# Performance work log

Measured on AMD Instinct MI355X. Metric: run time of the kernel, lower is better.

Reference implementation:

```python
import jax, jax.numpy as jnp
import numpy as np

N, H, S, R, T = 32768, 512, 8, 64, 12

def setup_inputs() -> dict:
    key = jax.random.key(0)
    ks = jax.random.split(key, 7)
    scale = 1.0 / np.sqrt(H)
    return {
        "encodings": jax.random.normal(ks[0], (N, H), dtype=jnp.float32),
        "domain_encs": jax.random.normal(ks[1], (S, H), dtype=jnp.float32),
        "Us": jax.random.normal(ks[2], (S, H, R), dtype=jnp.float32) * scale,
        "W1": jax.random.normal(ks[3], (S, H, H), dtype=jnp.float32) * scale,
        "b1": jax.random.normal(ks[4], (S, H), dtype=jnp.float32) * 0.01,
        "W2": jax.random.normal(ks[5], (S, H, T), dtype=jnp.float32) * scale,
        "b2": jax.random.normal(ks[6], (S, T), dtype=jnp.float32) * 0.01,
    }

def reference(encodings, domain_encs, Us, W1, b1, W2, b2):
    # Mahalanobis soft routing. Original computes (p-mu) @ (U U^T) @ (p-mu)^T
    # and takes sqrt(diag) -- algebraically identical to project-then-square-sum.
    diff = encodings[None, :, :] - domain_encs[:, None, :]        # [S, N, H]
    proj = jnp.einsum('snh,shr->snr', diff, Us)                   # [S, N, R]
    dist = jnp.sqrt(jnp.sum(proj * proj, axis=-1))                # [S, N]
    alphas = jax.nn.softmax(-dist, axis=0)                        # softmax over sources

    # Per-source classifier: Dropout(eval=identity) -> ReLU -> Linear(H,H)
    # -> Dropout -> ReLU -> Linear(H,T) -> Sigmoid
    h0 = jax.nn.relu(encodings)                                   # [N, H]
    h1 = jax.nn.relu(jnp.einsum('nh,shk->snk', h0, W1) + b1[:, None, :])  # [S, N, H]
    out = jax.nn.sigmoid(jnp.einsum('snk,skt->snt', h1, W2) + b2[:, None, :])  # [S, N, T]

    # Softmax-weighted combine of expert outputs
    return jnp.sum(alphas[:, :, None] * out, axis=0)              # [N, T]
```

## Files before the change

### kernel.cpp

```cpp
#include <hip/hip_runtime.h>
#include <hip/hip_bf16.h>

typedef unsigned short u16;
typedef __bf16 bf16x8 __attribute__((ext_vector_type(8)));
typedef float f32x4 __attribute__((ext_vector_type(4)));

#define NROWS 32768
#define H 512
#define NS 8
#define NR 64
#define NT 12

#define WS_W1T   0
#define WS_UCT   4194304
#define WS_W2T   4718592
#define WS_CVEC  4849664
#define WS_ALPH  4851712

union BFU { __bf16 h; u16 u; };
__device__ __forceinline__ u16 f2bf(float v) { BFU b; b.h = (__bf16)v; return b.u; }

__device__ __forceinline__ void gload16(const u16* g, u16* l) {
  __builtin_amdgcn_global_load_lds(
      (const __attribute__((address_space(1))) unsigned int*)g,
      (__attribute__((address_space(3))) unsigned int*)l, 16, 0, 0);
}

__global__ __launch_bounds__(256) void prep(
    const float* __restrict__ W1, u16* __restrict__ W1T,
    const float* __restrict__ Us, u16* __restrict__ UcatT,
    const float* __restrict__ W2, u16* __restrict__ W2T,
    const float* __restrict__ mu, float* __restrict__ cvec) {
  __shared__ float tile[32][33];
  const int bid = blockIdx.x;
  const int tx = threadIdx.x, ty = threadIdx.y;
  if (bid < 2432) {
    const float* in; u16* out; int Rr, Cc, Cpad, b, r0, c0;
    if (bid < 2048) {
      in = W1; out = W1T; Rr = 512; Cc = 512; Cpad = 512;
      r0 = (bid & 15) * 32; c0 = ((bid >> 4) & 15) * 32; b = bid >> 8;
    } else if (bid < 2304) {
      int t2 = bid - 2048; in = Us; out = UcatT; Rr = 512; Cc = 64; Cpad = 64;
      r0 = (t2 & 15) * 32; c0 = ((t2 >> 4) & 1) * 32; b = t2 >> 5;
    } else {
      int t2 = bid - 2304; in = W2; out = W2T; Rr = 512; Cc = 12; Cpad = 16;
      r0 = (t2 & 15) * 32; c0 = 0; b = t2 >> 4;
    }
#pragma unroll
    for (int i = 0; i < 4; i++) {
      int r = r0 + ty + i * 8, c = c0 + tx;
      float v = 0.f;
      if (r < Rr && c < Cc) v = in[((size_t)b * Rr + r) * Cc + c];
      tile[ty + i * 8][tx] = v;
    }
    __syncthreads();
#pragma unroll
    for (int i = 0; i < 4; i++) {
      int c = c0 + ty + i * 8, r = r0 + tx;
      if (c < Cpad && r < Rr) out[((size_t)b * Cpad + c) * Rr + r] = f2bf(tile[tx][ty + i * 8]);
    }
  } else {
    const int tid = ty * 32 + tx;
    const int idx = (bid - 2432) * 4 + (tid >> 6);
    const int s = idx >> 6, r = idx & 63, t = tid & 63;
    float acc = 0.f;
#pragma unroll
    for (int k = t; k < H; k += 64) acc += mu[s * H + k] * Us[((size_t)s * H + k) * NR + r];
#pragma unroll
    for (int m = 32; m; m >>= 1) acc += __shfl_xor(acc, m, 64);
    if (t == 0) cvec[idx] = acc;
  }
}

__device__ __forceinline__ void stageW16(const u16* __restrict__ g, u16* l, int tid) {
#pragma unroll
  for (int i = 0; i < 4; i++) {
    int flat = tid + i * 256;
    int r = flat >> 5, u = flat & 31;
    gload16(g + (size_t)r * 512 + (u ^ (r & 7)) * 8, l + flat * 8);
  }
}

__global__ __launch_bounds__(256, 2) void routing(
    const float* __restrict__ enc, const u16* __restrict__ UcatT,
    const float* __restrict__ cvec, float* __restrict__ alphT) {
  __shared__ __align__(16) u16 Wst[3][32 * 256];
  __shared__ float distS[NS][64];
  __shared__ float cvS[512];

  const int tid = threadIdx.x;
  const int wave = tid >> 6, lane = tid & 63;
  const int lnm = lane & 15, lnq = lane >> 4;
  const int row0 = blockIdx.x * 64;

  cvS[tid] = cvec[tid];
  cvS[256 + tid] = cvec[256 + tid];

  bf16x8 afrag[16];
  {
    const float* rp = enc + (size_t)(row0 + wave * 16 + lnm) * H + lnq * 8;
#pragma unroll
    for (int ks = 0; ks < 16; ks++) {
      float4 x0 = *(const float4*)(rp + ks * 32);
      float4 x1 = *(const float4*)(rp + ks * 32 + 4);
      bf16x8 a;
      a[0] = (__bf16)x0.x; a[1] = (__bf16)x0.y; a[2] = (__bf16)x0.z; a[3] = (__bf16)x0.w;
      a[4] = (__bf16)x1.x; a[5] = (__bf16)x1.y; a[6] = (__bf16)x1.z; a[7] = (__bf16)x1.w;
      afrag[ks] = a;
    }
  }

  __syncthreads();

  stageW16(UcatT, Wst[0], tid);
  int cb = 0;
  float dsq[4] = {0.f, 0.f, 0.f, 0.f};
#pragma unroll 1
  for (int wcw = 0; wcw < 16; wcw++) {
    f32x4 acc[2] = {};
#pragma unroll
    for (int kh = 0; kh < 2; kh++) {
      const int q = wcw * 2 + kh;
      const int nb = (cb == 2) ? 0 : cb + 1;
      if (q + 1 < 32) {
        stageW16(UcatT + (size_t)((q + 1) >> 1) * 32 * 512 + ((q + 1) & 1) * 256, Wst[nb], tid);
        asm volatile("s_waitcnt vmcnt(4)" ::: "memory");
      } else {
        asm volatile("s_waitcnt vmcnt(0)" ::: "memory");
      }
      __builtin_amdgcn_s_barrier();
      const u16* buf = Wst[cb];
#pragma unroll
      for (int ks = 0; ks < 8; ks++) {
        const int uu = ((ks * 4 + lnq) ^ (lnm & 7)) * 8;
        bf16x8 b0 = *(const bf16x8*)&buf[lnm * 256 + uu];
        bf16x8 b1v = *(const bf16x8*)&buf[(16 + lnm) * 256 + uu];
        acc[0] = __builtin_amdgcn_mfma_f32_16x16x32_bf16(afrag[kh * 8 + ks], b0, acc[0], 0, 0, 0);
        acc[1] = __builtin_amdgcn_mfma_f32_16x16x32_bf16(afrag[kh * 8 + ks], b1v, acc[1], 0, 0, 0);
      }
      cb = nb;
    }
#pragma unroll
    for (int ct = 0; ct < 2; ct++) {
      float cv = cvS[wcw * 32 + ct * 16 + lnm];
#pragma unroll
      for (int g = 0; g < 4; g++) { float d = acc[ct][g] - cv; dsq[g] += d * d; }
    }
    if (wcw & 1) {
#pragma unroll
      for (int m = 1; m < 16; m <<= 1) {
#pragma unroll
        for (int g = 0; g < 4; g++) dsq[g] += __shfl_xor(dsq[g], m, 16);
      }
      if (lnm == 0) {
#pragma unroll
        for (int g = 0; g < 4; g++) distS[wcw >> 1][wave * 16 + lnq * 4 + g] = sqrtf(dsq[g]);
      }
#pragma unroll
      for (int g = 0; g < 4; g++) dsq[g] = 0.f;
    }
  }
  __syncthreads();
  if (tid < 64) {
    float dmin = distS[0][tid];
#pragma unroll
    for (int s = 1; s < NS; s++) dmin = fminf(dmin, distS[s][tid]);
    float den = 0.f, e[NS];
#pragma unroll
    for (int s = 0; s < NS; s++) { e[s] = __expf(dmin - distS[s][tid]); den += e[s]; }
    float inv = 1.f / den;
#pragma unroll
    for (int s = 0; s < NS; s++) alphT[(size_t)s * NROWS + row0 + tid] = e[s] * inv;
  }
}

#define H1STR 40

__device__ __forceinline__ const u16* chunk_base(const u16* W1g, int q) {
  return W1g + ((size_t)(q >> 5) * 512 + ((q >> 1) & 15) * 32) * 512 + (q & 1) * 256;
}

__global__ __launch_bounds__(256, 2) void moe_main(
    const float* __restrict__ enc, const u16* __restrict__ W1T,
    const u16* __restrict__ W2T, const float* __restrict__ alphT,
    const float* __restrict__ b1g, const float* __restrict__ b2g,
    float* __restrict__ out) {
  __shared__ __align__(16) u16 Wst[3][32 * 256];
  __shared__ __align__(16) u16 h1c[128 * H1STR];
  __shared__ float alphS[4][128];

  const int tid = threadIdx.x;
  const int wave = tid >> 6, lane = tid & 63;
  const int lnm = lane & 15, lnq = lane >> 4;
  const int rb = blockIdx.x >> 1, sg = blockIdx.x & 1;
  const int row0 = rb * 128, sbase = sg * 4;

#pragma unroll
  for (int i = 0; i < 2; i++) {
    int u = tid + i * 256, j = u >> 7, r = u & 127;
    alphS[j][r] = alphT[(size_t)(sbase + j) * NROWS + row0 + r];
  }

  float b2v[4];
#pragma unroll
  for (int j = 0; j < 4; j++) b2v[j] = (lnm < NT) ? b2g[(sbase + j) * NT + lnm] : 0.f;

  bf16x8 efrag[2][16];
#pragma unroll
  for (int t = 0; t < 2; t++) {
    const float* rp = enc + (size_t)(row0 + wave * 32 + t * 16 + lnm) * H + lnq * 8;
#pragma unroll
    for (int ks = 0; ks < 16; ks++) {
      float4 x0 = *(const float4*)(rp + ks * 32);
      float4 x1 = *(const float4*)(rp + ks * 32 + 4);
      bf16x8 a;
      a[0] = (__bf16)fmaxf(x0.x, 0.f); a[1] = (__bf16)fmaxf(x0.y, 0.f);
      a[2] = (__bf16)fmaxf(x0.z, 0.f); a[3] = (__bf16)fmaxf(x0.w, 0.f);
      a[4] = (__bf16)fmaxf(x1.x, 0.f); a[5] = (__bf16)fmaxf(x1.y, 0.f);
      a[6] = (__bf16)fmaxf(x1.z, 0.f); a[7] = (__bf16)fmaxf(x1.w, 0.f);
      efrag[t][ks] = a;
    }
  }

  __syncthreads();

  const u16* W1g = W1T + (size_t)sbase * 512 * 512;
  stageW16(chunk_base(W1g, 0), Wst[0], tid);
  int cb = 0;
  f32x4 acc[2][2];
  float fin[2][4] = {};
#pragma unroll 1
  for (int j = 0; j < 4; j++) {
    const int s = sbase + j;
    f32x4 oacc[2] = {};
#pragma unroll 1
    for (int wc = 0; wc < 16; wc++) {
      const int q = j * 32 + wc * 2;
      float4 bq0 = *(const float4*)&b1g[s * H + wc * 32 + lnq * 4];
      float4 bq1 = *(const float4*)&b1g[s * H + wc * 32 + 16 + lnq * 4];
      bf16x8 bw = *(const bf16x8*)&W2T[((size_t)s * 16 + lnm) * H + wc * 32 + lnq * 8];
      asm volatile("" ::: "memory");
      {
        const int nb = (cb == 2) ? 0 : cb + 1;
        stageW16(chunk_base(W1g, q + 1), Wst[nb], tid);
        asm volatile("s_waitcnt vmcnt(7)" ::: "memory");
        __builtin_amdgcn_s_barrier();
        const u16* buf = Wst[cb];
#pragma unroll
        for (int t = 0; t < 2; t++) {
          acc[t][0] = (f32x4){bq0.x, bq0.y, bq0.z, bq0.w};
          acc[t][1] = (f32x4){bq1.x, bq1.y, bq1.z, bq1.w};
        }
#pragma unroll
        for (int ks = 0; ks < 8; ks++) {
          const int uu = ((ks * 4 + lnq) ^ (lnm & 7)) * 8;
          bf16x8 w0 = *(const bf16x8*)&buf[lnm * 256 + uu];
          bf16x8 w1 = *(const bf16x8*)&buf[(16 + lnm) * 256 + uu];
#pragma unroll
          for (int t = 0; t < 2; t++) {
            acc[t][0] = __builtin_amdgcn_mfma_f32_16x16x32_bf16(w0, efrag[t][ks], acc[t][0], 0, 0, 0);
            acc[t][1] = __builtin_amdgcn_mfma_f32_16x16x32_bf16(w1, efrag[t][ks], acc[t][1], 0, 0, 0);
          }
        }
        cb = nb;
      }
      {
        const int nb = (cb == 2) ? 0 : cb + 1;
        if (q + 2 < 128) {
          stageW16(chunk_base(W1g, q + 2), Wst[nb], tid);
          asm volatile("s_waitcnt vmcnt(4)" ::: "memory");
        } else {
          asm volatile("s_waitcnt vmcnt(0)" ::: "memory");
        }
        __builtin_amdgcn_s_barrier();
        const u16* buf = Wst[cb];
#pragma unroll
        for (int ks = 0; ks < 8; ks++) {
          const int uu = ((ks * 4 + lnq) ^ (lnm & 7)) * 8;
          bf16x8 w0 = *(const bf16x8*)&buf[lnm * 256 + uu];
          bf16x8 w1 = *(const bf16x8*)&buf[(16 + lnm) * 256 + uu];
#pragma unroll
          for (int t = 0; t < 2; t++) {
            acc[t][0] = __builtin_amdgcn_mfma_f32_16x16x32_bf16(w0, efrag[t][8 + ks], acc[t][0], 0, 0, 0);
            acc[t][1] = __builtin_amdgcn_mfma_f32_16x16x32_bf16(w1, efrag[t][8 + ks], acc[t][1], 0, 0, 0);
          }
        }
        cb = nb;
      }
#pragma unroll
      for (int ct = 0; ct < 2; ct++) {
#pragma unroll
        for (int t = 0; t < 2; t++) {
          union { u16 u[4]; uint2 v; } pk;
          pk.u[0] = f2bf(fmaxf(acc[t][ct][0], 0.f));
          pk.u[1] = f2bf(fmaxf(acc[t][ct][1], 0.f));
          pk.u[2] = f2bf(fmaxf(acc[t][ct][2], 0.f));
          pk.u[3] = f2bf(fmaxf(acc[t][ct][3], 0.f));
          *(uint2*)&h1c[(wave * 32 + t * 16 + lnm) * H1STR + ct * 16 + lnq * 4] = pk.v;
        }
      }
      {
#pragma unroll
        for (int t = 0; t < 2; t++) {
          bf16x8 a2 = *(const bf16x8*)&h1c[(wave * 32 + t * 16 + lnm) * H1STR + lnq * 8];
          oacc[t] = __builtin_amdgcn_mfma_f32_16x16x32_bf16(a2, bw, oacc[t], 0, 0, 0);
        }
      }
    }
    {
#pragma unroll
      for (int t = 0; t < 2; t++) {
#pragma unroll
        for (int g = 0; g < 4; g++) {
          float sig = 1.f / (1.f + __expf(-(oacc[t][g] + b2v[j])));
          fin[t][g] += alphS[j][wave * 32 + t * 16 + lnq * 4 + g] * sig;
        }
      }
    }
  }
  if (lnm < NT) {
#pragma unroll
    for (int t = 0; t < 2; t++) {
#pragma unroll
      for (int g = 0; g < 4; g++) {
        int rg = row0 + wave * 32 + t * 16 + lnq * 4 + g;
        atomicAdd(&out[(size_t)rg * NT + lnm], fin[t][g]);
      }
    }
  }
}

extern "C" void kernel_launch(void* const* d_in, const int* in_sizes, int n_in,
                              void* d_out, int out_size, void* d_ws, size_t ws_size,
                              hipStream_t stream) {
  const float* enc = (const float*)d_in[0];
  const float* mu  = (const float*)d_in[1];
  const float* Us  = (const float*)d_in[2];
  const float* W1  = (const float*)d_in[3];
  const float* b1  = (const float*)d_in[4];
  const float* W2  = (const float*)d_in[5];
  const float* b2  = (const float*)d_in[6];
  float* out = (float*)d_out;
  char* ws = (char*)d_ws;
  u16* W1T    = (u16*)(ws + WS_W1T);
  u16* UcatT  = (u16*)(ws + WS_UCT);
  u16* W2T    = (u16*)(ws + WS_W2T);
  float* cvec = (float*)(ws + WS_CVEC);
  float* alphT = (float*)(ws + WS_ALPH);

  prep<<<2560, dim3(32, 8, 1), 0, stream>>>(W1, W1T, Us, UcatT, W2, W2T, mu, cvec);
  routing<<<512, 256, 0, stream>>>(enc, UcatT, cvec, alphT);
  hipMemsetAsync(out, 0, (size_t)out_size * sizeof(float), stream);
  moe_main<<<512, 256, 0, stream>>>(enc, W1T, W2T, alphT, b1, b2, out);
}
```

Measured before the change: 270.1 us.

## Split routing by source groups over 128-row tiles and move softmax into moe_main

```diff
diff --git a/kernel.cpp b/kernel.cpp
--- a/kernel.cpp
+++ b/kernel.cpp
@@ -15,7 +15,7 @@
 #define WS_UCT   4194304
 #define WS_W2T   4718592
 #define WS_CVEC  4849664
-#define WS_ALPH  4851712
+#define WS_DIST  4851712
 
 union BFU { __bf16 h; u16 u; };
 __device__ __forceinline__ u16 f2bf(float v) { BFU b; b.h = (__bf16)v; return b.u; }
@@ -81,24 +81,29 @@
   }
 }
 
+__device__ __forceinline__ const u16* rchunk(const u16* U, int rcol0, int q) {
+  return U + ((size_t)(rcol0 + (q >> 2) * 64 + ((q >> 1) & 1) * 32)) * 512 + (q & 1) * 256;
+}
+
 __global__ __launch_bounds__(256, 2) void routing(
     const float* __restrict__ enc, const u16* __restrict__ UcatT,
-    const float* __restrict__ cvec, float* __restrict__ alphT) {
+    const float* __restrict__ cvec, float* __restrict__ distT) {
   __shared__ __align__(16) u16 Wst[3][32 * 256];
-  __shared__ float distS[NS][64];
-  __shared__ float cvS[512];
+  __shared__ float cvS[256];
 
   const int tid = threadIdx.x;
   const int wave = tid >> 6, lane = tid & 63;
   const int lnm = lane & 15, lnq = lane >> 4;
-  const int row0 = blockIdx.x * 64;
-
-  cvS[tid] = cvec[tid];
-  cvS[256 + tid] = cvec[256 + tid];
-
-  bf16x8 afrag[16];
-  {
-    const float* rp = enc + (size_t)(row0 + wave * 16 + lnm) * H + lnq * 8;
+  const int rb = blockIdx.x >> 1, sg = blockIdx.x & 1;
+  const int row0 = rb * 128, sbase = sg * 4;
+  const int rcol0 = sbase * 64;
+
+  cvS[tid] = cvec[rcol0 + tid];
+
+  bf16x8 efrag[2][16];
+#pragma unroll
+  for (int t = 0; t < 2; t++) {
+    const float* rp = enc + (size_t)(row0 + wave * 32 + t * 16 + lnm) * H + lnq * 8;
 #pragma unroll
     for (int ks = 0; ks < 16; ks++) {
       float4 x0 = *(const float4*)(rp + ks * 32);
@@ -106,71 +111,68 @@
       bf16x8 a;
       a[0] = (__bf16)x0.x; a[1] = (__bf16)x0.y; a[2] = (__bf16)x0.z; a[3] = (__bf16)x0.w;
       a[4] = (__bf16)x1.x; a[5] = (__bf16)x1.y; a[6] = (__bf16)x1.z; a[7] = (__bf16)x1.w;
-      afrag[ks] = a;
+      efrag[t][ks] = a;
     }
   }
 
   __syncthreads();
 
-  stageW16(UcatT, Wst[0], tid);
+  stageW16(rchunk(UcatT, rcol0, 0), Wst[0], tid);
   int cb = 0;
-  float dsq[4] = {0.f, 0.f, 0.f, 0.f};
+  f32x4 acc[2][2];
 #pragma unroll 1
-  for (int wcw = 0; wcw < 16; wcw++) {
-    f32x4 acc[2] = {};
-#pragma unroll
-    for (int kh = 0; kh < 2; kh++) {
-      const int q = wcw * 2 + kh;
-      const int nb = (cb == 2) ? 0 : cb + 1;
-      if (q + 1 < 32) {
-        stageW16(UcatT + (size_t)((q + 1) >> 1) * 32 * 512 + ((q + 1) & 1) * 256, Wst[nb], tid);
-        asm volatile("s_waitcnt vmcnt(4)" ::: "memory");
-      } else {
-        asm volatile("s_waitcnt vmcnt(0)" ::: "memory");
-      }
-      __builtin_amdgcn_s_barrier();
-      const u16* buf = Wst[cb];
-#pragma unroll
-      for (int ks = 0; ks < 8; ks++) {
-        const int uu = ((ks * 4 + lnq) ^ (lnm & 7)) * 8;
-        bf16x8 b0 = *(const bf16x8*)&buf[lnm * 256 + uu];
-        bf16x8 b1v = *(const bf16x8*)&buf[(16 + lnm) * 256 + uu];
-        acc[0] = __builtin_amdgcn_mfma_f32_16x16x32_bf16(afrag[kh * 8 + ks], b0, acc[0], 0, 0, 0);
-        acc[1] = __builtin_amdgcn_mfma_f32_16x16x32_bf16(afrag[kh * 8 + ks], b1v, acc[1], 0, 0, 0);
-      }
-      cb = nb;
-    }
-#pragma unroll
-    for (int ct = 0; ct < 2; ct++) {
-      float cv = cvS[wcw * 32 + ct * 16 + lnm];
-#pragma unroll
-      for (int g = 0; g < 4; g++) { float d = acc[ct][g] - cv; dsq[g] += d * d; }
-    }
-    if (wcw & 1) {
-#pragma unroll
-      for (int m = 1; m < 16; m <<= 1) {
-#pragma unroll
-        for (int g = 0; g < 4; g++) dsq[g] += __shfl_xor(dsq[g], m, 16);
-      }
-      if (lnm == 0) {
-#pragma unroll
-        for (int g = 0; g < 4; g++) distS[wcw >> 1][wave * 16 + lnq * 4 + g] = sqrtf(dsq[g]);
-      }
-#pragma unroll
-      for (int g = 0; g < 4; g++) dsq[g] = 0.f;
-    }
-  }
-  __syncthreads();
-  if (tid < 64) {
-    float dmin = distS[0][tid];
-#pragma unroll
-    for (int s = 1; s < NS; s++) dmin = fminf(dmin, distS[s][tid]);
-    float den = 0.f, e[NS];
-#pragma unroll
-    for (int s = 0; s < NS; s++) { e[s] = __expf(dmin - distS[s][tid]); den += e[s]; }
-    float inv = 1.f / den;
-#pragma unroll
-    for (int s = 0; s < NS; s++) alphT[(size_t)s * NROWS + row0 + tid] = e[s] * inv;
+  for (int j = 0; j < 4; j++) {
+    float dsq[2] = {0.f, 0.f};
+#pragma unroll 1
+    for (int wc = 0; wc < 2; wc++) {
+#pragma unroll
+      for (int t = 0; t < 2; t++) { acc[t][0] = (f32x4){0,0,0,0}; acc[t][1] = (f32x4){0,0,0,0}; }
+#pragma unroll
+      for (int kh = 0; kh < 2; kh++) {
+        const int q = j * 4 + wc * 2 + kh;
+        const int nb = (cb == 2) ? 0 : cb + 1;
+        if (q + 1 < 16) {
+          stageW16(rchunk(UcatT, rcol0, q + 1), Wst[nb], tid);
+          asm volatile("s_waitcnt vmcnt(4)" ::: "memory");
+        } else {
+          asm volatile("s_waitcnt vmcnt(0)" ::: "memory");
+        }
+        __builtin_amdgcn_s_barrier();
+        const u16* buf = Wst[cb];
+#pragma unroll
+        for (int ks = 0; ks < 8; ks++) {
+          const int uu = ((ks * 4 + lnq) ^ (lnm & 7)) * 8;
+          bf16x8 w0 = *(const bf16x8*)&buf[lnm * 256 + uu];
+          bf16x8 w1 = *(const bf16x8*)&buf[(16 + lnm) * 256 + uu];
+#pragma unroll
+          for (int t = 0; t < 2; t++) {
+            acc[t][0] = __builtin_amdgcn_mfma_f32_16x16x32_bf16(w0, efrag[t][kh * 8 + ks], acc[t][0], 0, 0, 0);
+            acc[t][1] = __builtin_amdgcn_mfma_f32_16x16x32_bf16(w1, efrag[t][kh * 8 + ks], acc[t][1], 0, 0, 0);
+          }
+        }
+        cb = nb;
+      }
+#pragma unroll
+      for (int ct = 0; ct < 2; ct++) {
+        float4 cv4 = *(const float4*)&cvS[j * 64 + wc * 32 + ct * 16 + lnq * 4];
+#pragma unroll
+        for (int t = 0; t < 2; t++) {
+          float d0 = acc[t][ct][0] - cv4.x, d1 = acc[t][ct][1] - cv4.y;
+          float d2 = acc[t][ct][2] - cv4.z, d3 = acc[t][ct][3] - cv4.w;
+          dsq[t] += d0 * d0 + d1 * d1 + d2 * d2 + d3 * d3;
+        }
+      }
+    }
+#pragma unroll
+    for (int t = 0; t < 2; t++) {
+      dsq[t] += __shfl_xor(dsq[t], 16, 64);
+      dsq[t] += __shfl_xor(dsq[t], 32, 64);
+    }
+    if (lnq == 0) {
+#pragma unroll
+      for (int t = 0; t < 2; t++)
+        distT[(size_t)(sbase + j) * NROWS + row0 + wave * 32 + t * 16 + lnm] = sqrtf(dsq[t]);
+    }
   }
 }
 
@@ -182,7 +184,7 @@
 
 __global__ __launch_bounds__(256, 2) void moe_main(
     const float* __restrict__ enc, const u16* __restrict__ W1T,
-    const u16* __restrict__ W2T, const float* __restrict__ alphT,
+    const u16* __restrict__ W2T, const float* __restrict__ distT,
     const float* __restrict__ b1g, const float* __restrict__ b2g,
     float* __restrict__ out) {
   __shared__ __align__(16) u16 Wst[3][32 * 256];
@@ -195,10 +197,19 @@
   const int rb = blockIdx.x >> 1, sg = blockIdx.x & 1;
   const int row0 = rb * 128, sbase = sg * 4;
 
-#pragma unroll
-  for (int i = 0; i < 2; i++) {
-    int u = tid + i * 256, j = u >> 7, r = u & 127;
-    alphS[j][r] = alphT[(size_t)(sbase + j) * NROWS + row0 + r];
+  if (tid < 128) {
+    float dv[NS], e[NS];
+#pragma unroll
+    for (int s2 = 0; s2 < NS; s2++) dv[s2] = distT[(size_t)s2 * NROWS + row0 + tid];
+    float dmin = dv[0];
+#pragma unroll
+    for (int s2 = 1; s2 < NS; s2++) dmin = fminf(dmin, dv[s2]);
+    float den = 0.f;
+#pragma unroll
+    for (int s2 = 0; s2 < NS; s2++) { e[s2] = __expf(dmin - dv[s2]); den += e[s2]; }
+    float inv = 1.f / den;
+#pragma unroll
+    for (int jj = 0; jj < 4; jj++) alphS[jj][tid] = e[sbase + jj] * inv;
   }
 
   float b2v[4];
@@ -346,10 +357,10 @@
   u16* UcatT  = (u16*)(ws + WS_UCT);
   u16* W2T    = (u16*)(ws + WS_W2T);
   float* cvec = (float*)(ws + WS_CVEC);
-  float* alphT = (float*)(ws + WS_ALPH);
+  float* distT = (float*)(ws + WS_DIST);
 
   prep<<<2560, dim3(32, 8, 1), 0, stream>>>(W1, W1T, Us, UcatT, W2, W2T, mu, cvec);
-  routing<<<512, 256, 0, stream>>>(enc, UcatT, cvec, alphT);
+  routing<<<512, 256, 0, stream>>>(enc, UcatT, cvec, distT);
   hipMemsetAsync(out, 0, (size_t)out_size * sizeof(float), stream);
-  moe_main<<<512, 256, 0, stream>>>(enc, W1T, W2T, alphT, b1, b2, out);
-}
+  moe_main<<<512, 256, 0, stream>>>(enc, W1T, W2T, distT, b1, b2, out);
+}
```

After: 268.3 us. No clear change (-0.7%).
